# Kernel tuning notes

Measured on AMD Instinct MI355X. Metric: run time of the kernel, lower is better.

The kernel has to match this reference:

```python
import jax, jax.numpy as jnp
import numpy as np

B, N, L, K = 32, 512, 8, 8


def setup_inputs() -> dict:
    key = jax.random.key(0)
    k1, k2 = jax.random.split(key)
    A = jax.random.normal(k1, (B, N, N), dtype=jnp.float32)
    A = 0.5 * (A + A.transpose(0, 2, 1))  # symmetric matrix, as in MMF use-case
    O_stack = jax.random.normal(k2, (L, B, K, K), dtype=jnp.float32)  # per-level KxK rotations
    rng = np.random.default_rng(0)
    idx = np.stack([np.sort(rng.choice(N, K, replace=False)) for _ in range(B * L)])
    indices = jnp.asarray(idx.reshape(B, L, K), dtype=jnp.int32)  # sorted, distinct per (b,l)
    wavelet = indices[:, :, 0]  # wavelet index is one of the selected indices per level
    return {"A": A, "O_stack": O_stack, "indices": indices, "wavelet": wavelet}


def reference(A, O_stack, indices, wavelet):
    Bz, Nz, _ = A.shape
    Lz = O_stack.shape[0]
    eye = jnp.eye(Nz, dtype=A.dtype)

    def build_U(idx, O):
        # identity except the KxK block at (idx_i, idx_j) replaced by O
        # (matches torch boolean-mask row-major fill since idx is sorted)
        return eye.at[idx[:, None], idx[None, :]].set(O)

    right = None
    for l in range(Lz):
        U = jax.vmap(build_U)(indices[:, l], O_stack[l])  # [B,N,N]
        right = U if l == 0 else U @ right
        A = U @ A @ U.transpose(0, 2, 1)

    # final masking: zero rows/cols of wavelet indices, keep diagonal
    active = jnp.ones((Bz, Nz), dtype=A.dtype).at[jnp.arange(Bz)[:, None], wavelet].set(0.0)
    left = active[:, :, None] * active[:, None, :]
    d = jnp.arange(Nz)
    left = left.at[:, d, d].set(1.0)
    D = A * left
    A_rec = right.transpose(0, 2, 1) @ D @ right
    return (A_rec, right, D)
```

## Files before the change

kernel.cpp:

```cpp
#include <hip/hip_runtime.h>

#define BATCH 32
#define NDIM 512
#define LNUM 8
#define KDIM 8

#define WS_PM     0
#define WS_S      512
#define WS_ACT    640
#define WS_W      1152
#define WS_B2     5248
#define WS_C2     9344
#define WS_RA     13440
#define WS_RD     46208
#define WS_STRIDE 78976

#define LSTR 65
#define ASTR 33

__global__ __launch_bounds__(256) void k_chain(
    const float* __restrict__ A, const float* __restrict__ O,
    const int* __restrict__ indices, const int* __restrict__ wavelet,
    float* __restrict__ ws)
{
    const int b = blockIdx.x;
    const int tid = threadIdx.x;
    float* base = ws + (size_t)b * WS_STRIDE;

    __shared__ float Wl[64*LSTR];
    __shared__ float P1[64*LSTR];
    __shared__ float P2[64*LSTR];
    __shared__ float B2l[64*LSTR];
    __shared__ int   pml[NDIM];
    __shared__ float actl[NDIM];
    __shared__ float actS[64];
    __shared__ int   idxsh[64];
    __shared__ int   Ssh[64];
    __shared__ int   prow[KDIM];
    __shared__ float Oall[LNUM*KDIM*KDIM];
    __shared__ int   s_sh;

    for (int t = tid; t < LNUM*KDIM*KDIM; t += 256) {
        int l = t >> 6, k = t & 63;
        Oall[t] = O[((size_t)l*BATCH + b)*(KDIM*KDIM) + k];
    }
    if (tid < 64) idxsh[tid] = indices[b*64 + tid];
    for (int n = tid; n < NDIM; n += 256) { pml[n] = -1; actl[n] = 1.f; }
    __syncthreads();

    if (tid < 64) {
        int n = idxsh[tid];
        bool first = true;
        for (int t = 0; t < tid; ++t) if (idxsh[t] == n) first = false;
        unsigned long long m = __ballot(first);
        int rank = __popcll(m & ((1ull << tid) - 1ull));
        if (first) { pml[n] = rank; Ssh[rank] = n; }
        if (tid == 0) s_sh = (int)__popcll(m);
    }
    if (tid >= 64 && tid < 64 + LNUM) {
        actl[wavelet[b*LNUM + (tid - 64)]] = 0.f;
    }
    __syncthreads();
    const int s = s_sh;
    if (tid < 64 && tid >= s) Ssh[tid] = 0;
    __syncthreads();
    if (tid < 64) actS[tid] = actl[Ssh[tid]];

    {
        int*   g_posmap = (int*)(base + WS_PM);
        int*   g_S      = (int*)(base + WS_S);
        float* g_act    = base + WS_ACT;
        for (int n = tid; n < NDIM; n += 256) { g_posmap[n] = pml[n]; g_act[n] = actl[n]; }
        if (tid < 64) g_S[tid] = Ssh[tid];
    }

    for (int t = tid; t < 4096; t += 256) {
        int rr = t >> 6, cc = t & 63;
        Wl[rr*LSTR + cc] = (rr == cc && rr < s) ? 1.f : 0.f;
    }
    __syncthreads();
    for (int l = 0; l < LNUM; ++l) {
        if (tid < KDIM) prow[tid] = pml[idxsh[l*KDIM + tid]];
        __syncthreads();
        for (int t = tid; t < KDIM*64; t += 256) {
            int i = t >> 6, c = t & 63;
            float acc = 0.f;
            #pragma unroll
            for (int j = 0; j < KDIM; ++j)
                acc += Oall[l*64 + i*KDIM + j] * Wl[prow[j]*LSTR + c];
            B2l[t] = acc;
        }
        __syncthreads();
        for (int t = tid; t < KDIM*64; t += 256) {
            int i = t >> 6, c = t & 63;
            Wl[prow[i]*LSTR + c] = B2l[t];
        }
        __syncthreads();
    }
    {
        float* g_W = base + WS_W;
        for (int t = tid; t < 4096; t += 256) g_W[t] = Wl[(t>>6)*LSTR + (t&63)];
    }

    for (int t = tid; t < 4096; t += 256) {
        int n = t >> 6, m = t & 63;
        P1[n*LSTR + m] = A[((size_t)b*NDIM + Ssh[n])*NDIM + Ssh[m]];
    }
    __syncthreads();

    const int w = tid >> 6;
    const int ln = tid & 63;
    float acc[16];

    #pragma unroll
    for (int k = 0; k < 16; ++k) acc[k] = 0.f;
    for (int n = 0; n < 64; ++n) {
        float as = P1[n*LSTR + ln];
        #pragma unroll
        for (int k = 0; k < 16; ++k) acc[k] += Wl[(w*16 + k)*LSTR + n] * as;
    }
    #pragma unroll
    for (int k = 0; k < 16; ++k) P2[(w*16 + k)*LSTR + ln] = acc[k];
    __syncthreads();

    #pragma unroll
    for (int k = 0; k < 16; ++k) acc[k] = 0.f;
    for (int m = 0; m < 64; ++m) {
        float wv = Wl[ln*LSTR + m];
        #pragma unroll
        for (int k = 0; k < 16; ++k) acc[k] += P2[(w*16 + k)*LSTR + m] * wv;
    }
    #pragma unroll
    for (int k = 0; k < 16; ++k) B2l[(w*16 + k)*LSTR + ln] = acc[k];
    __syncthreads();
    {
        float* g_B2 = base + WS_B2;
        for (int t = tid; t < 4096; t += 256) g_B2[t] = B2l[(t>>6)*LSTR + (t&63)];
    }

    for (int t = tid; t < 4096; t += 256) {
        int n = t >> 6, m = t & 63;
        float mv = (Ssh[n] == Ssh[m]) ? 1.f : actS[n]*actS[m];
        P1[n*LSTR + m] = mv * B2l[n*LSTR + m];
    }
    __syncthreads();

    #pragma unroll
    for (int k = 0; k < 16; ++k) acc[k] = 0.f;
    for (int n = 0; n < 64; ++n) {
        float dv = P1[n*LSTR + ln];
        #pragma unroll
        for (int k = 0; k < 16; ++k) acc[k] += Wl[n*LSTR + (w*16 + k)] * dv;
    }
    #pragma unroll
    for (int k = 0; k < 16; ++k) P2[(w*16 + k)*LSTR + ln] = acc[k];
    __syncthreads();

    #pragma unroll
    for (int k = 0; k < 16; ++k) acc[k] = 0.f;
    for (int m = 0; m < 64; ++m) {
        float wv = Wl[m*LSTR + ln];
        #pragma unroll
        for (int k = 0; k < 16; ++k) acc[k] += P2[(w*16 + k)*LSTR + m] * wv;
    }
    {
        float* g_C2 = base + WS_C2;
        #pragma unroll
        for (int k = 0; k < 16; ++k) g_C2[(w*16 + k)*64 + ln] = acc[k];
    }
}

__global__ __launch_bounds__(256) void k_rard(const float* __restrict__ A,
                                              float* __restrict__ ws)
{
    const int b = blockIdx.x;
    const int j0 = blockIdx.y * 32;
    const int tid = threadIdx.x;
    float* base = ws + (size_t)b * WS_STRIDE;
    const int*   g_S   = (const int*)(base + WS_S);
    const float* g_act = base + WS_ACT;
    const float* g_W   = base + WS_W;
    float* g_RA = base + WS_RA;
    float* g_RD = base + WS_RD;

    __shared__ float Wl[64*LSTR];
    __shared__ float AS[64*ASTR];
    __shared__ float RAt[64*ASTR];
    __shared__ int   Ssh[64];
    __shared__ float actS[64];
    __shared__ float actc[32];

    for (int t = tid; t < 4096; t += 256)
        Wl[(t>>6)*LSTR + (t&63)] = g_W[t];
    if (tid < 64) {
        int n = g_S[tid];
        Ssh[tid] = n;
        actS[tid] = g_act[n];
    }
    if (tid >= 64 && tid < 96) actc[tid-64] = g_act[j0 + (tid-64)];
    __syncthreads();

    for (int t = tid; t < 2048; t += 256) {
        int n = t >> 5, c = t & 31;
        AS[n*ASTR + c] = A[((size_t)b*NDIM + Ssh[n])*NDIM + j0 + c];
    }
    __syncthreads();

    const int c = tid & 31;
    const int g = tid >> 5;
    float acc[8];

    #pragma unroll
    for (int k = 0; k < 8; ++k) acc[k] = 0.f;
    for (int n = 0; n < 64; ++n) {
        float av = AS[n*ASTR + c];
        #pragma unroll
        for (int k = 0; k < 8; ++k) acc[k] += Wl[(g*8 + k)*LSTR + n] * av;
    }
    #pragma unroll
    for (int k = 0; k < 8; ++k) {
        RAt[(g*8 + k)*ASTR + c] = acc[k];
        g_RA[(g*8 + k)*NDIM + j0 + c] = acc[k];
    }
    __syncthreads();

    const float actj = actc[c];
    #pragma unroll
    for (int k = 0; k < 8; ++k) acc[k] = 0.f;
    for (int n = 0; n < 64; ++n) {
        float dv = actS[n] * actj * RAt[n*ASTR + c];
        #pragma unroll
        for (int k = 0; k < 8; ++k) acc[k] += Wl[n*LSTR + g*8 + k] * dv;
    }
    #pragma unroll
    for (int k = 0; k < 8; ++k)
        g_RD[(g*8 + k)*NDIM + j0 + c] = acc[k];
}

__global__ __launch_bounds__(256) void k_big(const float* __restrict__ A,
                                             const float* __restrict__ ws,
                                             float* __restrict__ out)
{
    const int b = blockIdx.y;
    const int rh = threadIdx.x >> 7;
    const int lane = threadIdx.x & 127;
    const int i = blockIdx.x*2 + rh;
    const int j0 = lane*4;

    const float* base = ws + (size_t)b * WS_STRIDE;
    const int*   posmap = (const int*)(base + WS_PM);
    const float* act = base + WS_ACT;
    const float* g_W  = base + WS_W;
    const float* g_B2 = base + WS_B2;
    const float* g_C2 = base + WS_C2;
    const float* RA = base + WS_RA;
    const float* RD = base + WS_RD;

    const int pi = posmap[i];
    const float acti = act[i];
    const size_t rowoff = ((size_t)b*NDIM + i)*NDIM;
    const size_t seg = (size_t)BATCH*NDIM*NDIM;

    int4   p4  = ((const int4*)posmap)[lane];
    float4 aj4 = ((const float4*)act)[lane];
    int   pm[4] = {p4.x, p4.y, p4.z, p4.w};
    float aj[4] = {aj4.x, aj4.y, aj4.z, aj4.w};

    float a[4], arec[4], dv[4], rv[4];

    if (pi < 0) {
        float4 v = ((const float4*)(A + rowoff))[lane];
        a[0]=v.x; a[1]=v.y; a[2]=v.z; a[3]=v.w;
        #pragma unroll
        for (int c = 0; c < 4; ++c) {
            int pj = pm[c];
            if (pj >= 0) a[c] = RA[pj*NDIM + i];
            float mv = (i == j0 + c) ? 1.f : acti * aj[c];
            dv[c] = a[c] * mv;
            arec[c] = (pj < 0) ? dv[c] : RD[pj*NDIM + i];
            rv[c] = (i == j0 + c) ? 1.f : 0.f;
        }
    } else {
        float4 v = ((const float4*)(RA + pi*NDIM))[lane];
        float4 w = ((const float4*)(RD + pi*NDIM))[lane];
        a[0]=v.x; a[1]=v.y; a[2]=v.z; a[3]=v.w;
        arec[0]=w.x; arec[1]=w.y; arec[2]=w.z; arec[3]=w.w;
        #pragma unroll
        for (int c = 0; c < 4; ++c) {
            int pj = pm[c];
            if (pj >= 0) {
                a[c]    = g_B2[pi*64 + pj];
                arec[c] = g_C2[pi*64 + pj];
                rv[c]   = g_W[pi*64 + pj];
            } else {
                rv[c] = 0.f;
            }
            float mv = (i == j0 + c) ? 1.f : acti * aj[c];
            dv[c] = a[c] * mv;
        }
    }

    ((float4*)(out + rowoff))[lane]         = make_float4(arec[0], arec[1], arec[2], arec[3]);
    ((float4*)(out + seg + rowoff))[lane]   = make_float4(rv[0], rv[1], rv[2], rv[3]);
    ((float4*)(out + 2*seg + rowoff))[lane] = make_float4(dv[0], dv[1], dv[2], dv[3]);
}

extern "C" void kernel_launch(void* const* d_in, const int* in_sizes, int n_in,
                              void* d_out, int out_size, void* d_ws, size_t ws_size,
                              hipStream_t stream) {
    const float* A       = (const float*)d_in[0];
    const float* O       = (const float*)d_in[1];
    const int*   indices = (const int*)d_in[2];
    const int*   wavelet = (const int*)d_in[3];
    float* ws  = (float*)d_ws;
    float* out = (float*)d_out;

    k_chain<<<dim3(BATCH), 256, 0, stream>>>(A, O, indices, wavelet, ws);
    k_rard <<<dim3(BATCH, 16), 256, 0, stream>>>(A, ws);
    k_big  <<<dim3(NDIM/2, BATCH), 256, 0, stream>>>(A, ws, out);
}
```

Measured before the change: 196.7 us.

## Merge chain and row-projection kernels into one prep kernel; nontemporal output stores

Folds k_chain and k_rard into a single k_prep launch over a (batch, 17) grid. Every block recomputes the small W chain redundantly, then part 16 does the 64x64 sandwich products and parts 0-15 compute the RA/RD column slabs. This removes one kernel launch and the serialized single-block-per-batch chain phase that the row kernels used to wait on. The cost is redundant chain work in every block and more shared memory per block. The final kernel's output writes also switch to nontemporal vector stores to reduce cache pollution.

Measured after the change: 197.3 us. Within noise of the previous version (+0.3%).

```diff
diff --git a/kernel.cpp b/kernel.cpp
--- a/kernel.cpp
+++ b/kernel.cpp
@@ -18,19 +18,20 @@
 #define LSTR 65
 #define ASTR 33
 
-__global__ __launch_bounds__(256) void k_chain(
+typedef float f4 __attribute__((ext_vector_type(4)));
+
+__global__ __launch_bounds__(256) void k_prep(
     const float* __restrict__ A, const float* __restrict__ O,
     const int* __restrict__ indices, const int* __restrict__ wavelet,
     float* __restrict__ ws)
 {
     const int b = blockIdx.x;
+    const int part = blockIdx.y;
     const int tid = threadIdx.x;
     float* base = ws + (size_t)b * WS_STRIDE;
 
     __shared__ float Wl[64*LSTR];
-    __shared__ float P1[64*LSTR];
-    __shared__ float P2[64*LSTR];
-    __shared__ float B2l[64*LSTR];
+    __shared__ float pool[3*64*LSTR];
     __shared__ int   pml[NDIM];
     __shared__ float actl[NDIM];
     __shared__ float actS[64];
@@ -66,14 +67,6 @@
     __syncthreads();
     if (tid < 64) actS[tid] = actl[Ssh[tid]];
 
-    {
-        int*   g_posmap = (int*)(base + WS_PM);
-        int*   g_S      = (int*)(base + WS_S);
-        float* g_act    = base + WS_ACT;
-        for (int n = tid; n < NDIM; n += 256) { g_posmap[n] = pml[n]; g_act[n] = actl[n]; }
-        if (tid < 64) g_S[tid] = Ssh[tid];
-    }
-
     for (int t = tid; t < 4096; t += 256) {
         int rr = t >> 6, cc = t & 63;
         Wl[rr*LSTR + cc] = (rr == cc && rr < s) ? 1.f : 0.f;
@@ -88,153 +81,140 @@
             #pragma unroll
             for (int j = 0; j < KDIM; ++j)
                 acc += Oall[l*64 + i*KDIM + j] * Wl[prow[j]*LSTR + c];
-            B2l[t] = acc;
+            pool[t] = acc;
         }
         __syncthreads();
         for (int t = tid; t < KDIM*64; t += 256) {
             int i = t >> 6, c = t & 63;
-            Wl[prow[i]*LSTR + c] = B2l[t];
-        }
-        __syncthreads();
-    }
-    {
-        float* g_W = base + WS_W;
-        for (int t = tid; t < 4096; t += 256) g_W[t] = Wl[(t>>6)*LSTR + (t&63)];
-    }
-
-    for (int t = tid; t < 4096; t += 256) {
-        int n = t >> 6, m = t & 63;
-        P1[n*LSTR + m] = A[((size_t)b*NDIM + Ssh[n])*NDIM + Ssh[m]];
-    }
-    __syncthreads();
-
-    const int w = tid >> 6;
-    const int ln = tid & 63;
-    float acc[16];
-
-    #pragma unroll
-    for (int k = 0; k < 16; ++k) acc[k] = 0.f;
-    for (int n = 0; n < 64; ++n) {
-        float as = P1[n*LSTR + ln];
-        #pragma unroll
-        for (int k = 0; k < 16; ++k) acc[k] += Wl[(w*16 + k)*LSTR + n] * as;
-    }
-    #pragma unroll
-    for (int k = 0; k < 16; ++k) P2[(w*16 + k)*LSTR + ln] = acc[k];
-    __syncthreads();
-
-    #pragma unroll
-    for (int k = 0; k < 16; ++k) acc[k] = 0.f;
-    for (int m = 0; m < 64; ++m) {
-        float wv = Wl[ln*LSTR + m];
-        #pragma unroll
-        for (int k = 0; k < 16; ++k) acc[k] += P2[(w*16 + k)*LSTR + m] * wv;
-    }
-    #pragma unroll
-    for (int k = 0; k < 16; ++k) B2l[(w*16 + k)*LSTR + ln] = acc[k];
-    __syncthreads();
-    {
-        float* g_B2 = base + WS_B2;
-        for (int t = tid; t < 4096; t += 256) g_B2[t] = B2l[(t>>6)*LSTR + (t&63)];
-    }
-
-    for (int t = tid; t < 4096; t += 256) {
-        int n = t >> 6, m = t & 63;
-        float mv = (Ssh[n] == Ssh[m]) ? 1.f : actS[n]*actS[m];
-        P1[n*LSTR + m] = mv * B2l[n*LSTR + m];
-    }
-    __syncthreads();
-
-    #pragma unroll
-    for (int k = 0; k < 16; ++k) acc[k] = 0.f;
-    for (int n = 0; n < 64; ++n) {
-        float dv = P1[n*LSTR + ln];
-        #pragma unroll
-        for (int k = 0; k < 16; ++k) acc[k] += Wl[n*LSTR + (w*16 + k)] * dv;
-    }
-    #pragma unroll
-    for (int k = 0; k < 16; ++k) P2[(w*16 + k)*LSTR + ln] = acc[k];
-    __syncthreads();
-
-    #pragma unroll
-    for (int k = 0; k < 16; ++k) acc[k] = 0.f;
-    for (int m = 0; m < 64; ++m) {
-        float wv = Wl[m*LSTR + ln];
-        #pragma unroll
-        for (int k = 0; k < 16; ++k) acc[k] += P2[(w*16 + k)*LSTR + m] * wv;
-    }
-    {
-        float* g_C2 = base + WS_C2;
-        #pragma unroll
-        for (int k = 0; k < 16; ++k) g_C2[(w*16 + k)*64 + ln] = acc[k];
-    }
-}
-
-__global__ __launch_bounds__(256) void k_rard(const float* __restrict__ A,
-                                              float* __restrict__ ws)
-{
-    const int b = blockIdx.x;
-    const int j0 = blockIdx.y * 32;
-    const int tid = threadIdx.x;
-    float* base = ws + (size_t)b * WS_STRIDE;
-    const int*   g_S   = (const int*)(base + WS_S);
-    const float* g_act = base + WS_ACT;
-    const float* g_W   = base + WS_W;
-    float* g_RA = base + WS_RA;
-    float* g_RD = base + WS_RD;
-
-    __shared__ float Wl[64*LSTR];
-    __shared__ float AS[64*ASTR];
-    __shared__ float RAt[64*ASTR];
-    __shared__ int   Ssh[64];
-    __shared__ float actS[64];
-    __shared__ float actc[32];
-
-    for (int t = tid; t < 4096; t += 256)
-        Wl[(t>>6)*LSTR + (t&63)] = g_W[t];
-    if (tid < 64) {
-        int n = g_S[tid];
-        Ssh[tid] = n;
-        actS[tid] = g_act[n];
-    }
-    if (tid >= 64 && tid < 96) actc[tid-64] = g_act[j0 + (tid-64)];
-    __syncthreads();
-
-    for (int t = tid; t < 2048; t += 256) {
-        int n = t >> 5, c = t & 31;
-        AS[n*ASTR + c] = A[((size_t)b*NDIM + Ssh[n])*NDIM + j0 + c];
-    }
-    __syncthreads();
-
-    const int c = tid & 31;
-    const int g = tid >> 5;
-    float acc[8];
-
-    #pragma unroll
-    for (int k = 0; k < 8; ++k) acc[k] = 0.f;
-    for (int n = 0; n < 64; ++n) {
-        float av = AS[n*ASTR + c];
-        #pragma unroll
-        for (int k = 0; k < 8; ++k) acc[k] += Wl[(g*8 + k)*LSTR + n] * av;
-    }
-    #pragma unroll
-    for (int k = 0; k < 8; ++k) {
-        RAt[(g*8 + k)*ASTR + c] = acc[k];
-        g_RA[(g*8 + k)*NDIM + j0 + c] = acc[k];
-    }
-    __syncthreads();
-
-    const float actj = actc[c];
-    #pragma unroll
-    for (int k = 0; k < 8; ++k) acc[k] = 0.f;
-    for (int n = 0; n < 64; ++n) {
-        float dv = actS[n] * actj * RAt[n*ASTR + c];
-        #pragma unroll
-        for (int k = 0; k < 8; ++k) acc[k] += Wl[n*LSTR + g*8 + k] * dv;
-    }
-    #pragma unroll
-    for (int k = 0; k < 8; ++k)
-        g_RD[(g*8 + k)*NDIM + j0 + c] = acc[k];
+            Wl[prow[i]*LSTR + c] = pool[t];
+        }
+        __syncthreads();
+    }
+
+    if (part == 16) {
+        float* P1  = pool;
+        float* P2  = pool + 64*LSTR;
+        float* B2l = pool + 2*64*LSTR;
+
+        {
+            int*   g_posmap = (int*)(base + WS_PM);
+            int*   g_S      = (int*)(base + WS_S);
+            float* g_act    = base + WS_ACT;
+            float* g_W      = base + WS_W;
+            for (int n = tid; n < NDIM; n += 256) { g_posmap[n] = pml[n]; g_act[n] = actl[n]; }
+            if (tid < 64) g_S[tid] = Ssh[tid];
+            for (int t = tid; t < 4096; t += 256) g_W[t] = Wl[(t>>6)*LSTR + (t&63)];
+        }
+
+        for (int t = tid; t < 4096; t += 256) {
+            int n = t >> 6, m = t & 63;
+            P1[n*LSTR + m] = A[((size_t)b*NDIM + Ssh[n])*NDIM + Ssh[m]];
+        }
+        __syncthreads();
+
+        const int w = tid >> 6;
+        const int ln = tid & 63;
+        float acc[16];
+
+        #pragma unroll
+        for (int k = 0; k < 16; ++k) acc[k] = 0.f;
+        for (int n = 0; n < 64; ++n) {
+            float as = P1[n*LSTR + ln];
+            #pragma unroll
+            for (int k = 0; k < 16; ++k) acc[k] += Wl[(w*16 + k)*LSTR + n] * as;
+        }
+        #pragma unroll
+        for (int k = 0; k < 16; ++k) P2[(w*16 + k)*LSTR + ln] = acc[k];
+        __syncthreads();
+
+        #pragma unroll
+        for (int k = 0; k < 16; ++k) acc[k] = 0.f;
+        for (int m = 0; m < 64; ++m) {
+            float wv = Wl[ln*LSTR + m];
+            #pragma unroll
+            for (int k = 0; k < 16; ++k) acc[k] += P2[(w*16 + k)*LSTR + m] * wv;
+        }
+        #pragma unroll
+        for (int k = 0; k < 16; ++k) B2l[(w*16 + k)*LSTR + ln] = acc[k];
+        __syncthreads();
+        {
+            float* g_B2 = base + WS_B2;
+            for (int t = tid; t < 4096; t += 256) g_B2[t] = B2l[(t>>6)*LSTR + (t&63)];
+        }
+
+        for (int t = tid; t < 4096; t += 256) {
+            int n = t >> 6, m = t & 63;
+            float mv = (Ssh[n] == Ssh[m]) ? 1.f : actS[n]*actS[m];
+            P1[n*LSTR + m] = mv * B2l[n*LSTR + m];
+        }
+        __syncthreads();
+
+        #pragma unroll
+        for (int k = 0; k < 16; ++k) acc[k] = 0.f;
+        for (int n = 0; n < 64; ++n) {
+            float dv = P1[n*LSTR + ln];
+            #pragma unroll
+            for (int k = 0; k < 16; ++k) acc[k] += Wl[n*LSTR + (w*16 + k)] * dv;
+        }
+        #pragma unroll
+        for (int k = 0; k < 16; ++k) P2[(w*16 + k)*LSTR + ln] = acc[k];
+        __syncthreads();
+
+        #pragma unroll
+        for (int k = 0; k < 16; ++k) acc[k] = 0.f;
+        for (int m = 0; m < 64; ++m) {
+            float wv = Wl[m*LSTR + ln];
+            #pragma unroll
+            for (int k = 0; k < 16; ++k) acc[k] += P2[(w*16 + k)*LSTR + m] * wv;
+        }
+        {
+            float* g_C2 = base + WS_C2;
+            #pragma unroll
+            for (int k = 0; k < 16; ++k) g_C2[(w*16 + k)*64 + ln] = acc[k];
+        }
+    } else {
+        float* AS  = pool;
+        float* RAt = pool + 64*ASTR;
+        float* g_RA = base + WS_RA;
+        float* g_RD = base + WS_RD;
+        const int j0 = part * 32;
+
+        for (int t = tid; t < 2048; t += 256) {
+            int n = t >> 5, c = t & 31;
+            AS[n*ASTR + c] = A[((size_t)b*NDIM + Ssh[n])*NDIM + j0 + c];
+        }
+        __syncthreads();
+
+        const int c = tid & 31;
+        const int g = tid >> 5;
+        float acc[8];
+
+        #pragma unroll
+        for (int k = 0; k < 8; ++k) acc[k] = 0.f;
+        for (int n = 0; n < 64; ++n) {
+            float av = AS[n*ASTR + c];
+            #pragma unroll
+            for (int k = 0; k < 8; ++k) acc[k] += Wl[(g*8 + k)*LSTR + n] * av;
+        }
+        #pragma unroll
+        for (int k = 0; k < 8; ++k) {
+            RAt[(g*8 + k)*ASTR + c] = acc[k];
+            g_RA[(g*8 + k)*NDIM + j0 + c] = acc[k];
+        }
+        __syncthreads();
+
+        const float actj = actl[j0 + c];
+        #pragma unroll
+        for (int k = 0; k < 8; ++k) acc[k] = 0.f;
+        for (int n = 0; n < 64; ++n) {
+            float dv = actS[n] * actj * RAt[n*ASTR + c];
+            #pragma unroll
+            for (int k = 0; k < 8; ++k) acc[k] += Wl[n*LSTR + g*8 + k] * dv;
+        }
+        #pragma unroll
+        for (int k = 0; k < 8; ++k)
+            g_RD[(g*8 + k)*NDIM + j0 + c] = acc[k];
+    }
 }
 
 __global__ __launch_bounds__(256) void k_big(const float* __restrict__ A,
@@ -300,9 +280,12 @@
         }
     }
 
-    ((float4*)(out + rowoff))[lane]         = make_float4(arec[0], arec[1], arec[2], arec[3]);
-    ((float4*)(out + seg + rowoff))[lane]   = make_float4(rv[0], rv[1], rv[2], rv[3]);
-    ((float4*)(out + 2*seg + rowoff))[lane] = make_float4(dv[0], dv[1], dv[2], dv[3]);
+    f4 v0 = { arec[0], arec[1], arec[2], arec[3] };
+    f4 v1 = { rv[0],   rv[1],   rv[2],   rv[3]   };
+    f4 v2 = { dv[0],   dv[1],   dv[2],   dv[3]   };
+    __builtin_nontemporal_store(v0, (f4*)(out + rowoff) + lane);
+    __builtin_nontemporal_store(v1, (f4*)(out + seg + rowoff) + lane);
+    __builtin_nontemporal_store(v2, (f4*)(out + 2*seg + rowoff) + lane);
 }
 
 extern "C" void kernel_launch(void* const* d_in, const int* in_sizes, int n_in,
@@ -315,7 +298,6 @@
     float* ws  = (float*)d_ws;
     float* out = (float*)d_out;
 
-    k_chain<<<dim3(BATCH), 256, 0, stream>>>(A, O, indices, wavelet, ws);
-    k_rard <<<dim3(BATCH, 16), 256, 0, stream>>>(A, ws);
-    k_big  <<<dim3(NDIM/2, BATCH), 256, 0, stream>>>(A, ws, out);
+    k_prep<<<dim3(BATCH, 17), 256, 0, stream>>>(A, O, indices, wavelet, ws);
+    k_big <<<dim3(NDIM/2, BATCH), 256, 0, stream>>>(A, ws, out);
 }
```

## Fuse RA/RD computation into output kernel, eliminating workspace round-trip

Applied to the files above, without the earlier changes.

The separate k_rard kernel and the RA/RD global workspace buffers are removed. The output kernel now handles two cases. Blocks for non-selected rows recompute their 64 RA/RD entries from the A row in shared memory. Extra blocks per batch compute the selected-row panels directly and write them out. This drops one launch and the global write-then-read of intermediates, and adds nontemporal stores, in exchange for redundant small matmuls per row block.

Measured after the change: 209.5 us. 1.06x slower.

```diff
diff --git a/kernel.cpp b/kernel.cpp
--- a/kernel.cpp
+++ b/kernel.cpp
@@ -7,18 +7,17 @@
 
 #define WS_PM     0
 #define WS_S      512
+#define WS_SCNT   576
 #define WS_ACT    640
 #define WS_W      1152
 #define WS_B2     5248
 #define WS_C2     9344
-#define WS_RA     13440
-#define WS_RD     46208
 #define WS_STRIDE 78976
 
 #define LSTR 65
-#define ASTR 33
-
-__global__ __launch_bounds__(256) void k_chain(
+typedef float f4 __attribute__((ext_vector_type(4)));
+
+__global__ __launch_bounds__(256) void k_small(
     const float* __restrict__ A, const float* __restrict__ O,
     const int* __restrict__ indices, const int* __restrict__ wavelet,
     float* __restrict__ ws)
@@ -72,6 +71,7 @@
         float* g_act    = base + WS_ACT;
         for (int n = tid; n < NDIM; n += 256) { g_posmap[n] = pml[n]; g_act[n] = actl[n]; }
         if (tid < 64) g_S[tid] = Ssh[tid];
+        if (tid == 0) ((int*)(base + WS_SCNT))[0] = s;
     }
 
     for (int t = tid; t < 4096; t += 256) {
@@ -170,139 +170,165 @@
     }
 }
 
-__global__ __launch_bounds__(256) void k_rard(const float* __restrict__ A,
-                                              float* __restrict__ ws)
+__global__ __launch_bounds__(256) void k_out(const float* __restrict__ A,
+                                             const float* __restrict__ ws,
+                                             float* __restrict__ out)
 {
-    const int b = blockIdx.x;
-    const int j0 = blockIdx.y * 32;
+    const int part = blockIdx.x;
+    const int b = blockIdx.y;
     const int tid = threadIdx.x;
-    float* base = ws + (size_t)b * WS_STRIDE;
+    const float* base = ws + (size_t)b * WS_STRIDE;
+    const int*   g_pm  = (const int*)(base + WS_PM);
     const int*   g_S   = (const int*)(base + WS_S);
     const float* g_act = base + WS_ACT;
     const float* g_W   = base + WS_W;
-    float* g_RA = base + WS_RA;
-    float* g_RD = base + WS_RD;
+    const float* g_B2  = base + WS_B2;
+    const float* g_C2  = base + WS_C2;
+    const int scnt = ((const int*)(base + WS_SCNT))[0];
+    const size_t seg = (size_t)BATCH*NDIM*NDIM;
 
     __shared__ float Wl[64*LSTR];
-    __shared__ float AS[64*ASTR];
-    __shared__ float RAt[64*ASTR];
+    __shared__ float pool[2*64*LSTR];
     __shared__ int   Ssh[64];
     __shared__ float actS[64];
-    __shared__ float actc[32];
-
-    for (int t = tid; t < 4096; t += 256)
-        Wl[(t>>6)*LSTR + (t&63)] = g_W[t];
-    if (tid < 64) {
-        int n = g_S[tid];
-        Ssh[tid] = n;
-        actS[tid] = g_act[n];
-    }
-    if (tid >= 64 && tid < 96) actc[tid-64] = g_act[j0 + (tid-64)];
-    __syncthreads();
-
-    for (int t = tid; t < 2048; t += 256) {
-        int n = t >> 5, c = t & 31;
-        AS[n*ASTR + c] = A[((size_t)b*NDIM + Ssh[n])*NDIM + j0 + c];
-    }
-    __syncthreads();
-
-    const int c = tid & 31;
-    const int g = tid >> 5;
-    float acc[8];
-
-    #pragma unroll
-    for (int k = 0; k < 8; ++k) acc[k] = 0.f;
-    for (int n = 0; n < 64; ++n) {
-        float av = AS[n*ASTR + c];
-        #pragma unroll
-        for (int k = 0; k < 8; ++k) acc[k] += Wl[(g*8 + k)*LSTR + n] * av;
-    }
-    #pragma unroll
-    for (int k = 0; k < 8; ++k) {
-        RAt[(g*8 + k)*ASTR + c] = acc[k];
-        g_RA[(g*8 + k)*NDIM + j0 + c] = acc[k];
-    }
-    __syncthreads();
-
-    const float actj = actc[c];
-    #pragma unroll
-    for (int k = 0; k < 8; ++k) acc[k] = 0.f;
-    for (int n = 0; n < 64; ++n) {
-        float dv = actS[n] * actj * RAt[n*ASTR + c];
-        #pragma unroll
-        for (int k = 0; k < 8; ++k) acc[k] += Wl[n*LSTR + g*8 + k] * dv;
-    }
-    #pragma unroll
-    for (int k = 0; k < 8; ++k)
-        g_RD[(g*8 + k)*NDIM + j0 + c] = acc[k];
-}
-
-__global__ __launch_bounds__(256) void k_big(const float* __restrict__ A,
-                                             const float* __restrict__ ws,
-                                             float* __restrict__ out)
-{
-    const int b = blockIdx.y;
-    const int rh = threadIdx.x >> 7;
-    const int lane = threadIdx.x & 127;
-    const int i = blockIdx.x*2 + rh;
-    const int j0 = lane*4;
-
-    const float* base = ws + (size_t)b * WS_STRIDE;
-    const int*   posmap = (const int*)(base + WS_PM);
-    const float* act = base + WS_ACT;
-    const float* g_W  = base + WS_W;
-    const float* g_B2 = base + WS_B2;
-    const float* g_C2 = base + WS_C2;
-    const float* RA = base + WS_RA;
-    const float* RD = base + WS_RD;
-
-    const int pi = posmap[i];
-    const float acti = act[i];
-    const size_t rowoff = ((size_t)b*NDIM + i)*NDIM;
-    const size_t seg = (size_t)BATCH*NDIM*NDIM;
-
-    int4   p4  = ((const int4*)posmap)[lane];
-    float4 aj4 = ((const float4*)act)[lane];
-    int   pm[4] = {p4.x, p4.y, p4.z, p4.w};
-    float aj[4] = {aj4.x, aj4.y, aj4.z, aj4.w};
-
-    float a[4], arec[4], dv[4], rv[4];
-
-    if (pi < 0) {
-        float4 v = ((const float4*)(A + rowoff))[lane];
-        a[0]=v.x; a[1]=v.y; a[2]=v.z; a[3]=v.w;
-        #pragma unroll
-        for (int c = 0; c < 4; ++c) {
-            int pj = pm[c];
-            if (pj >= 0) a[c] = RA[pj*NDIM + i];
-            float mv = (i == j0 + c) ? 1.f : acti * aj[c];
-            dv[c] = a[c] * mv;
-            arec[c] = (pj < 0) ? dv[c] : RD[pj*NDIM + i];
-            rv[c] = (i == j0 + c) ? 1.f : 0.f;
+    __shared__ int   pmj[64];
+    __shared__ float actj[64];
+
+    if (tid < 64) { int s = g_S[tid]; Ssh[tid] = s; actS[tid] = g_act[s]; }
+    for (int t = tid; t < 1024; t += 256) {
+        f4 w = ((const f4*)g_W)[t];
+        int r = t >> 4, c = (t & 15) * 4;
+        Wl[r*LSTR + c]   = w.x; Wl[r*LSTR + c+1] = w.y;
+        Wl[r*LSTR + c+2] = w.z; Wl[r*LSTR + c+3] = w.w;
+    }
+
+    if (part < NDIM/4) {
+        float* rowbuf = pool;
+        float* ArowS  = pool + 2048;
+        float* ras    = pool + 2048 + 256;
+        float* rds    = pool + 2048 + 512;
+        const int r = tid >> 6;
+        const int c = tid & 63;
+        const int i = part*4 + r;
+        const int pi = g_pm[i];
+        const float acti = g_act[i];
+        const float* Arow = A + ((size_t)b*NDIM + i)*NDIM;
+
+        f4 a0 = ((const f4*)Arow)[2*c];
+        f4 a1 = ((const f4*)Arow)[2*c + 1];
+        ((f4*)(rowbuf + r*512))[2*c]     = a0;
+        ((f4*)(rowbuf + r*512))[2*c + 1] = a1;
+        __syncthreads();
+
+        ArowS[r*64 + c] = rowbuf[r*512 + Ssh[c]];
+        __syncthreads();
+
+        {
+            float acc = 0.f;
+            #pragma unroll 8
+            for (int k = 0; k < 64; ++k)
+                acc += Wl[c*LSTR + k] * ArowS[r*64 + k];
+            ras[r*64 + c] = acc;
+        }
+        __syncthreads();
+
+        {
+            float acc = 0.f;
+            #pragma unroll 8
+            for (int n = 0; n < 64; ++n)
+                acc += Wl[n*LSTR + c] * (actS[n] * ras[r*64 + n]);
+            rds[r*64 + c] = acc * acti;
+        }
+        __syncthreads();
+
+        if (pi < 0) {
+            int4   p0 = ((const int4*)g_pm)[2*c],  p1 = ((const int4*)g_pm)[2*c + 1];
+            float4 q0 = ((const float4*)g_act)[2*c], q1 = ((const float4*)g_act)[2*c + 1];
+            int   pm8[8] = {p0.x,p0.y,p0.z,p0.w, p1.x,p1.y,p1.z,p1.w};
+            float aj8[8] = {q0.x,q0.y,q0.z,q0.w, q1.x,q1.y,q1.z,q1.w};
+            float av8[8] = {a0.x,a0.y,a0.z,a0.w, a1.x,a1.y,a1.z,a1.w};
+            float arec[8], dvv[8], rvv[8];
+            const int j0 = 8*c;
+            #pragma unroll
+            for (int e = 0; e < 8; ++e) {
+                int pj = pm8[e];
+                int j = j0 + e;
+                float a  = (pj >= 0) ? ras[r*64 + pj] : av8[e];
+                float mv = (i == j) ? 1.f : acti * aj8[e];
+                dvv[e]  = a * mv;
+                arec[e] = (pj >= 0) ? rds[r*64 + pj] : dvv[e];
+                rvv[e]  = (i == j) ? 1.f : 0.f;
+            }
+            const size_t ro = ((size_t)b*NDIM + i)*NDIM;
+            f4 s0 = {arec[0],arec[1],arec[2],arec[3]};
+            f4 s1 = {arec[4],arec[5],arec[6],arec[7]};
+            f4 s2 = {rvv[0],rvv[1],rvv[2],rvv[3]};
+            f4 s3 = {rvv[4],rvv[5],rvv[6],rvv[7]};
+            f4 s4 = {dvv[0],dvv[1],dvv[2],dvv[3]};
+            f4 s5 = {dvv[4],dvv[5],dvv[6],dvv[7]};
+            __builtin_nontemporal_store(s0, (f4*)(out + ro) + 2*c);
+            __builtin_nontemporal_store(s1, (f4*)(out + ro) + 2*c + 1);
+            __builtin_nontemporal_store(s2, (f4*)(out + seg + ro) + 2*c);
+            __builtin_nontemporal_store(s3, (f4*)(out + seg + ro) + 2*c + 1);
+            __builtin_nontemporal_store(s4, (f4*)(out + 2*seg + ro) + 2*c);
+            __builtin_nontemporal_store(s5, (f4*)(out + 2*seg + ro) + 2*c + 1);
         }
     } else {
-        float4 v = ((const float4*)(RA + pi*NDIM))[lane];
-        float4 w = ((const float4*)(RD + pi*NDIM))[lane];
-        a[0]=v.x; a[1]=v.y; a[2]=v.z; a[3]=v.w;
-        arec[0]=w.x; arec[1]=w.y; arec[2]=w.z; arec[3]=w.w;
-        #pragma unroll
-        for (int c = 0; c < 4; ++c) {
-            int pj = pm[c];
-            if (pj >= 0) {
-                a[c]    = g_B2[pi*64 + pj];
-                arec[c] = g_C2[pi*64 + pj];
-                rv[c]   = g_W[pi*64 + pj];
-            } else {
-                rv[c] = 0.f;
-            }
-            float mv = (i == j0 + c) ? 1.f : acti * aj[c];
-            dv[c] = a[c] * mv;
-        }
-    }
-
-    ((float4*)(out + rowoff))[lane]         = make_float4(arec[0], arec[1], arec[2], arec[3]);
-    ((float4*)(out + seg + rowoff))[lane]   = make_float4(rv[0], rv[1], rv[2], rv[3]);
-    ((float4*)(out + 2*seg + rowoff))[lane] = make_float4(dv[0], dv[1], dv[2], dv[3]);
+        const int j0 = (part - NDIM/4) * 64;
+        float* AS  = pool;
+        float* RAt = pool + 4096;
+        if (tid < 64) { pmj[tid] = g_pm[j0 + tid]; actj[tid] = g_act[j0 + tid]; }
+        __syncthreads();
+        for (int t = tid; t < 1024; t += 256) {
+            int n = t >> 4, cc = (t & 15) * 4;
+            f4 v = ((const f4*)(A + ((size_t)b*NDIM + Ssh[n])*NDIM + j0))[t & 15];
+            AS[n*64 + cc]   = v.x; AS[n*64 + cc+1] = v.y;
+            AS[n*64 + cc+2] = v.z; AS[n*64 + cc+3] = v.w;
+        }
+        __syncthreads();
+
+        const int g = tid >> 6;
+        const int j = tid & 63;
+        float racc[16];
+
+        #pragma unroll
+        for (int k = 0; k < 16; ++k) racc[k] = 0.f;
+        for (int n = 0; n < 64; ++n) {
+            float av = AS[n*64 + j];
+            #pragma unroll
+            for (int k = 0; k < 16; ++k) racc[k] += Wl[(g*16 + k)*LSTR + n] * av;
+        }
+        #pragma unroll
+        for (int k = 0; k < 16; ++k) RAt[(g*16 + k)*64 + j] = racc[k];
+        __syncthreads();
+
+        #pragma unroll
+        for (int k = 0; k < 16; ++k) racc[k] = 0.f;
+        for (int n = 0; n < 64; ++n) {
+            float dt = actS[n] * RAt[n*64 + j];
+            #pragma unroll
+            for (int k = 0; k < 16; ++k) racc[k] += Wl[n*LSTR + g*16 + k] * dt;
+        }
+
+        const int   pjv = pmj[j];
+        const float ajv = actj[j];
+        #pragma unroll
+        for (int k = 0; k < 16; ++k) {
+            int m = g*16 + k;
+            if (m >= scnt) continue;
+            int Sm = Ssh[m];
+            float rdv  = racc[k] * ajv;
+            float arec = (pjv < 0) ? rdv : g_C2[m*64 + pjv];
+            float afin = (pjv < 0) ? RAt[m*64 + j] : g_B2[m*64 + pjv];
+            float mask = (Sm == j0 + j) ? 1.f : actS[m] * ajv;
+            float dvv  = afin * mask;
+            float rvv  = (pjv < 0) ? 0.f : Wl[m*LSTR + pjv];
+            size_t ro = ((size_t)b*NDIM + Sm)*NDIM + j0 + j;
+            __builtin_nontemporal_store(arec, out + ro);
+            __builtin_nontemporal_store(rvv,  out + seg + ro);
+            __builtin_nontemporal_store(dvv,  out + 2*seg + ro);
+        }
+    }
 }
 
 extern "C" void kernel_launch(void* const* d_in, const int* in_sizes, int n_in,
@@ -315,7 +341,6 @@
     float* ws  = (float*)d_ws;
     float* out = (float*)d_out;
 
-    k_chain<<<dim3(BATCH), 256, 0, stream>>>(A, O, indices, wavelet, ws);
-    k_rard <<<dim3(BATCH, 16), 256, 0, stream>>>(A, ws);
-    k_big  <<<dim3(NDIM/2, BATCH), 256, 0, stream>>>(A, ws, out);
+    k_small<<<dim3(BATCH), 256, 0, stream>>>(A, O, indices, wavelet, ws);
+    k_out  <<<dim3(NDIM/4 + 8, BATCH), 256, 0, stream>>>(A, ws, out);
 }
```

## Store transposed RA/RD copies so k_big reads selected columns contiguously

Applied to the files above, without the earlier changes.

The middle kernel now handles 64-column tiles with 16 outputs per thread and vectorized loads. It also writes transposed copies of RA and RD into new workspace regions. In the large output kernel, rows outside the selected set now read their gathered RA/RD values from a contiguous 64-float row of the transposed arrays, replacing strided column accesses with NDIM stride. The cost is extra global writes in the middle kernel, a larger workspace, and fewer blocks for the middle stage.

After: 187.6 us. 4.6% less time.

```diff
diff --git a/kernel.cpp b/kernel.cpp
--- a/kernel.cpp
+++ b/kernel.cpp
@@ -13,12 +13,14 @@
 #define WS_C2     9344
 #define WS_RA     13440
 #define WS_RD     46208
-#define WS_STRIDE 78976
+#define WS_RAT    78976
+#define WS_RDT    111744
+#define WS_STRIDE 144512
 
 #define LSTR 65
-#define ASTR 33
-
-__global__ __launch_bounds__(256) void k_chain(
+typedef float f4 __attribute__((ext_vector_type(4)));
+
+__global__ __launch_bounds__(256) void k_small(
     const float* __restrict__ A, const float* __restrict__ O,
     const int* __restrict__ indices, const int* __restrict__ wavelet,
     float* __restrict__ ws)
@@ -170,71 +172,98 @@
     }
 }
 
-__global__ __launch_bounds__(256) void k_rard(const float* __restrict__ A,
-                                              float* __restrict__ ws)
+__global__ __launch_bounds__(256) void k_mid(const float* __restrict__ A,
+                                             float* __restrict__ ws)
 {
     const int b = blockIdx.x;
-    const int j0 = blockIdx.y * 32;
+    const int j0 = blockIdx.y * 64;
     const int tid = threadIdx.x;
     float* base = ws + (size_t)b * WS_STRIDE;
     const int*   g_S   = (const int*)(base + WS_S);
     const float* g_act = base + WS_ACT;
     const float* g_W   = base + WS_W;
-    float* g_RA = base + WS_RA;
-    float* g_RD = base + WS_RD;
+    float* g_RA  = base + WS_RA;
+    float* g_RD  = base + WS_RD;
+    float* g_RAT = base + WS_RAT;
+    float* g_RDT = base + WS_RDT;
 
     __shared__ float Wl[64*LSTR];
-    __shared__ float AS[64*ASTR];
-    __shared__ float RAt[64*ASTR];
+    __shared__ float AS[64*64];
+    __shared__ float RAt[64*64];
     __shared__ int   Ssh[64];
     __shared__ float actS[64];
-    __shared__ float actc[32];
-
-    for (int t = tid; t < 4096; t += 256)
-        Wl[(t>>6)*LSTR + (t&63)] = g_W[t];
+    __shared__ float actj[64];
+
+    for (int t = tid; t < 1024; t += 256) {
+        f4 w = ((const f4*)g_W)[t];
+        int r = t >> 4, c = (t & 15) * 4;
+        Wl[r*LSTR + c]   = w.x; Wl[r*LSTR + c+1] = w.y;
+        Wl[r*LSTR + c+2] = w.z; Wl[r*LSTR + c+3] = w.w;
+    }
     if (tid < 64) {
         int n = g_S[tid];
         Ssh[tid] = n;
         actS[tid] = g_act[n];
     }
-    if (tid >= 64 && tid < 96) actc[tid-64] = g_act[j0 + (tid-64)];
-    __syncthreads();
-
-    for (int t = tid; t < 2048; t += 256) {
-        int n = t >> 5, c = t & 31;
-        AS[n*ASTR + c] = A[((size_t)b*NDIM + Ssh[n])*NDIM + j0 + c];
-    }
-    __syncthreads();
-
-    const int c = tid & 31;
-    const int g = tid >> 5;
-    float acc[8];
-
-    #pragma unroll
-    for (int k = 0; k < 8; ++k) acc[k] = 0.f;
+    if (tid >= 64 && tid < 128) actj[tid-64] = g_act[j0 + (tid-64)];
+    __syncthreads();
+
+    for (int t = tid; t < 1024; t += 256) {
+        int n = t >> 4, cc = (t & 15) * 4;
+        f4 v = ((const f4*)(A + ((size_t)b*NDIM + Ssh[n])*NDIM + j0))[t & 15];
+        AS[n*64 + cc]   = v.x; AS[n*64 + cc+1] = v.y;
+        AS[n*64 + cc+2] = v.z; AS[n*64 + cc+3] = v.w;
+    }
+    __syncthreads();
+
+    const int g = tid >> 6;
+    const int j = tid & 63;
+    float racc[16];
+
+    #pragma unroll
+    for (int k = 0; k < 16; ++k) racc[k] = 0.f;
     for (int n = 0; n < 64; ++n) {
-        float av = AS[n*ASTR + c];
-        #pragma unroll
-        for (int k = 0; k < 8; ++k) acc[k] += Wl[(g*8 + k)*LSTR + n] * av;
-    }
-    #pragma unroll
-    for (int k = 0; k < 8; ++k) {
-        RAt[(g*8 + k)*ASTR + c] = acc[k];
-        g_RA[(g*8 + k)*NDIM + j0 + c] = acc[k];
-    }
-    __syncthreads();
-
-    const float actj = actc[c];
-    #pragma unroll
-    for (int k = 0; k < 8; ++k) acc[k] = 0.f;
+        float av = AS[n*64 + j];
+        #pragma unroll
+        for (int k = 0; k < 16; ++k) racc[k] += Wl[(g*16 + k)*LSTR + n] * av;
+    }
+    #pragma unroll
+    for (int k = 0; k < 16; ++k) {
+        RAt[(g*16 + k)*64 + j] = racc[k];
+        g_RA[(g*16 + k)*NDIM + j0 + j] = racc[k];
+    }
+    {
+        f4* dst = (f4*)(g_RAT + (size_t)(j0 + j)*64 + g*16);
+        #pragma unroll
+        for (int q = 0; q < 4; ++q) {
+            f4 v = { racc[4*q], racc[4*q+1], racc[4*q+2], racc[4*q+3] };
+            dst[q] = v;
+        }
+    }
+    __syncthreads();
+
+    #pragma unroll
+    for (int k = 0; k < 16; ++k) racc[k] = 0.f;
     for (int n = 0; n < 64; ++n) {
-        float dv = actS[n] * actj * RAt[n*ASTR + c];
-        #pragma unroll
-        for (int k = 0; k < 8; ++k) acc[k] += Wl[n*LSTR + g*8 + k] * dv;
-    }
-    #pragma unroll
-    for (int k = 0; k < 8; ++k)
-        g_RD[(g*8 + k)*NDIM + j0 + c] = acc[k];
+        float dt = actS[n] * RAt[n*64 + j];
+        #pragma unroll
+        for (int k = 0; k < 16; ++k) racc[k] += Wl[n*LSTR + g*16 + k] * dt;
+    }
+    const float aj = actj[j];
+    #pragma unroll
+    for (int k = 0; k < 16; ++k) {
+        float rd = racc[k] * aj;
+        racc[k] = rd;
+        g_RD[(g*16 + k)*NDIM + j0 + j] = rd;
+    }
+    {
+        f4* dst = (f4*)(g_RDT + (size_t)(j0 + j)*64 + g*16);
+        #pragma unroll
+        for (int q = 0; q < 4; ++q) {
+            f4 v = { racc[4*q], racc[4*q+1], racc[4*q+2], racc[4*q+3] };
+            dst[q] = v;
+        }
+    }
 }
 
 __global__ __launch_bounds__(256) void k_big(const float* __restrict__ A,
@@ -253,8 +282,10 @@
     const float* g_W  = base + WS_W;
     const float* g_B2 = base + WS_B2;
     const float* g_C2 = base + WS_C2;
-    const float* RA = base + WS_RA;
-    const float* RD = base + WS_RD;
+    const float* RA  = base + WS_RA;
+    const float* RD  = base + WS_RD;
+    const float* RAT = base + WS_RAT;
+    const float* RDT = base + WS_RDT;
 
     const int pi = posmap[i];
     const float acti = act[i];
@@ -269,20 +300,22 @@
     float a[4], arec[4], dv[4], rv[4];
 
     if (pi < 0) {
+        const float* rat = RAT + (size_t)i*64;
+        const float* rdt = RDT + (size_t)i*64;
         float4 v = ((const float4*)(A + rowoff))[lane];
         a[0]=v.x; a[1]=v.y; a[2]=v.z; a[3]=v.w;
         #pragma unroll
         for (int c = 0; c < 4; ++c) {
             int pj = pm[c];
-            if (pj >= 0) a[c] = RA[pj*NDIM + i];
+            if (pj >= 0) a[c] = rat[pj];
             float mv = (i == j0 + c) ? 1.f : acti * aj[c];
             dv[c] = a[c] * mv;
-            arec[c] = (pj < 0) ? dv[c] : RD[pj*NDIM + i];
+            arec[c] = (pj < 0) ? dv[c] : rdt[pj];
             rv[c] = (i == j0 + c) ? 1.f : 0.f;
         }
     } else {
-        float4 v = ((const float4*)(RA + pi*NDIM))[lane];
-        float4 w = ((const float4*)(RD + pi*NDIM))[lane];
+        float4 v = ((const float4*)(RA + (size_t)pi*NDIM))[lane];
+        float4 w = ((const float4*)(RD + (size_t)pi*NDIM))[lane];
         a[0]=v.x; a[1]=v.y; a[2]=v.z; a[3]=v.w;
         arec[0]=w.x; arec[1]=w.y; arec[2]=w.z; arec[3]=w.w;
         #pragma unroll
@@ -315,7 +348,7 @@
     float* ws  = (float*)d_ws;
     float* out = (float*)d_out;
 
-    k_chain<<<dim3(BATCH), 256, 0, stream>>>(A, O, indices, wavelet, ws);
-    k_rard <<<dim3(BATCH, 16), 256, 0, stream>>>(A, ws);
+    k_small<<<dim3(BATCH), 256, 0, stream>>>(A, O, indices, wavelet, ws);
+    k_mid  <<<dim3(BATCH, 8), 256, 0, stream>>>(A, ws);
     k_big  <<<dim3(NDIM/2, BATCH), 256, 0, stream>>>(A, ws, out);
 }
```
